# Performance work log

Measured on AMD Instinct MI355X. Metric: run time of the kernel, lower is better.

Reference implementation:

```python
import jax, jax.numpy as jnp
import numpy as np
from jax import lax

DEPTH, HEADS, DH, DIM, M, V, NUM_EMB, D_VQ = 6, 8, 64, 512, 256, 523, 512, 64


def _ln(x, g, b):
    mu = jnp.mean(x, -1, keepdims=True)
    var = jnp.var(x, -1, keepdims=True)
    return (x - mu) * lax.rsqrt(var + 1e-5) * g + b


def _softmax_kernel(data, proj, is_query):
    # FAVOR+ positive softmax features (performer-pytorch softmax_kernel)
    dn = data * (data.shape[-1] ** -0.25)
    dd = jnp.einsum('bhld,md->bhlm', dn, proj)
    diag = 0.5 * jnp.sum(dn * dn, axis=-1, keepdims=True)
    mx = jnp.max(dd, axis=-1, keepdims=True) if is_query else jnp.max(dd)
    return jnp.exp(dd - diag - lax.stop_gradient(mx)) * (proj.shape[0] ** -0.5) + 1e-4


def _causal_linear_attn(qp, kp, v):
    # out_t = qp_t . cumsum_t(kp v^T) / (qp_t . cumsum_t(kp))
    kc = jnp.cumsum(kp, axis=2)
    den = jnp.einsum('bhlm,bhlm->bhl', qp, kc)
    kv = jnp.cumsum(jnp.einsum('bhlm,bhld->bhlmd', kp, v), axis=2)
    return jnp.einsum('bhlm,bhlmd->bhld', qp, kv) / den[..., None]


def _vq_encode(_x, conv1_w, conv1_b, conv2_w, conv2_b, codebook):
    dn = ('NCDHW', 'OIDHW', 'NCDHW')
    h = lax.conv_general_dilated(_x, conv1_w, (2, 2, 2), [(1, 1)] * 3, dimension_numbers=dn)
    h = jax.nn.relu(h + conv1_b[None, :, None, None, None])
    h = lax.conv_general_dilated(h, conv2_w, (2, 2, 2), [(1, 1)] * 3, dimension_numbers=dn)
    h = h + conv2_b[None, :, None, None, None]                 # [N, D, 4,4,4]
    z = jnp.transpose(h, (0, 2, 3, 4, 1))                      # [N, 4,4,4, D]
    flat = z.reshape(-1, z.shape[-1])
    d2 = (jnp.sum(flat * flat, 1, keepdims=True)
          - 2.0 * flat @ codebook.T
          + jnp.sum(codebook * codebook, 1)[None, :])
    inds = jnp.argmin(d2, axis=1).astype(jnp.int32)
    return inds.reshape(z.shape[:4])                           # [N, 4,4,4]


def _performer_loss(seq, tok_emb, pos_emb, proj, ln1_g, ln1_b, wq, wk, wv, wo, bo,
                    ln2_g, ln2_b, ff1_w, ff1_b, ff2_w, ff2_b, lnf_g, lnf_b,
                    logits_w, logits_b):
    inp, tgt = seq[:, :-1], seq[:, 1:]
    b, L = inp.shape
    h = tok_emb[inp] + pos_emb[:L][None]
    split = lambda t: jnp.transpose(t.reshape(b, L, HEADS, DH), (0, 2, 1, 3))
    for l in range(DEPTH):
        x1 = _ln(h, ln1_g[l], ln1_b[l])
        q, k, v = split(x1 @ wq[l]), split(x1 @ wk[l]), split(x1 @ wv[l])
        qp = _softmax_kernel(q, proj[l], True)
        kp = _softmax_kernel(k, proj[l], False)
        o = _causal_linear_attn(qp, kp, v)
        o = jnp.transpose(o, (0, 2, 1, 3)).reshape(b, L, DIM)
        h = h + o @ wo[l] + bo[l]
        x2 = _ln(h, ln2_g[l], ln2_b[l])
        h = h + jax.nn.gelu(x2 @ ff1_w[l] + ff1_b[l]) @ ff2_w[l] + ff2_b[l]
    h = _ln(h, lnf_g, lnf_b)
    logits = h @ logits_w + logits_b
    lp = jax.nn.log_softmax(logits, axis=-1)
    nll = -jnp.take_along_axis(lp, tgt[..., None], axis=-1)[..., 0]
    return jnp.mean(nll)


def setup_inputs() -> dict:
    key = jax.random.key(0)
    ks = jax.random.split(key, 24)
    n = lambda k, sh, s=0.02: (jax.random.normal(k, sh) * s).astype(jnp.float32)
    bs = 16
    return {
        'x': jax.random.normal(ks[0], (bs, 1, 16, 16, 16), jnp.float32),
        'xn': jax.random.normal(ks[1], (bs, 1, 1, 16, 16, 16), jnp.float32),
        'i': jax.random.randint(ks[2], (bs, 3), 0, V, jnp.int32),
        # frozen VQ-VAE
        'conv1_w': n(ks[3], (32, 1, 4, 4, 4), 0.1), 'conv1_b': jnp.zeros((32,), jnp.float32),
        'conv2_w': n(ks[4], (D_VQ, 32, 4, 4, 4), 0.05), 'conv2_b': jnp.zeros((D_VQ,), jnp.float32),
        'codebook': jax.random.normal(ks[5], (NUM_EMB, D_VQ), jnp.float32),
        # FAVOR+ random-feature projections (non-trainable buffer)
        'proj': jax.random.normal(ks[6], (DEPTH, M, DH), jnp.float32),
        # performer params
        'tok_emb': n(ks[7], (V, DIM)), 'pos_emb': n(ks[8], (131, DIM)),
        'ln1_g': jnp.ones((DEPTH, DIM), jnp.float32), 'ln1_b': jnp.zeros((DEPTH, DIM), jnp.float32),
        'wq': n(ks[9], (DEPTH, DIM, DIM)), 'wk': n(ks[10], (DEPTH, DIM, DIM)),
        'wv': n(ks[11], (DEPTH, DIM, DIM)), 'wo': n(ks[12], (DEPTH, DIM, DIM)),
        'bo': jnp.zeros((DEPTH, DIM), jnp.float32),
        'ln2_g': jnp.ones((DEPTH, DIM), jnp.float32), 'ln2_b': jnp.zeros((DEPTH, DIM), jnp.float32),
        'ff1_w': n(ks[13], (DEPTH, DIM, 4 * DIM)), 'ff1_b': jnp.zeros((DEPTH, 4 * DIM), jnp.float32),
        'ff2_w': n(ks[14], (DEPTH, 4 * DIM, DIM)), 'ff2_b': jnp.zeros((DEPTH, DIM), jnp.float32),
        'lnf_g': jnp.ones((DIM,), jnp.float32), 'lnf_b': jnp.zeros((DIM,), jnp.float32),
        'logits_w': n(ks[15], (DIM, V)), 'logits_b': jnp.zeros((V,), jnp.float32),
    }


def reference(x, xn, i, conv1_w, conv1_b, conv2_w, conv2_b, codebook, proj,
              tok_emb, pos_emb, ln1_g, ln1_b, wq, wk, wv, wo, bo, ln2_g, ln2_b,
              ff1_w, ff1_b, ff2_w, ff2_b, lnf_g, lnf_b, logits_w, logits_b):
    bs = x.shape[0]
    _xn = xn.reshape((-1,) + xn.shape[2:])            # (b n) c x y z
    _x = jnp.concatenate([x, _xn], axis=0)
    inds = _vq_encode(_x, conv1_w, conv1_b, conv2_w, conv2_b, codebook)
    inds_i = inds[:bs].reshape(bs, -1)                # b (x y z)
    inds_r = inds[bs:].reshape(bs, -1)                # b (n x y z)
    seq = jnp.concatenate([i.astype(jnp.int32), inds_r, inds_i], axis=1)  # [b, 131]
    return _performer_loss(seq, tok_emb, pos_emb, proj, ln1_g, ln1_b, wq, wk, wv, wo,
                           bo, ln2_g, ln2_b, ff1_w, ff1_b, ff2_w, ff2_b,
                           lnf_g, lnf_b, logits_w, logits_b)
```

## Files before the change

### kernel.cpp

```cpp
#include <hip/hip_runtime.h>

#define SEQL 130
#define LSEQ 131
#define DIMM 512
#define NHEADS 8
#define MF 256
#define VSZ 523
#define NROWS (16*SEQL)
#define NBH (16*NHEADS)
#define NBHL (NBH*SEQL)
#define QSEG 1064960
#define WLAYER 3145728

typedef __attribute__((ext_vector_type(8))) short short8;
typedef __attribute__((ext_vector_type(8))) unsigned short us8;
typedef __attribute__((ext_vector_type(4))) unsigned short us4;
typedef __attribute__((ext_vector_type(4))) float f32x4;

__device__ __forceinline__ unsigned short f2bf(float f){
  unsigned int u = __float_as_uint(f);
  u += 0x7fffu + ((u>>16)&1u);
  return (unsigned short)(u>>16);
}
__device__ __forceinline__ float bf2f(unsigned short h){
  return __uint_as_float(((unsigned int)h)<<16);
}
__device__ __forceinline__ float gelu_f(float x){
  float x3 = x*x*x;
  return 0.5f*x*(1.f+tanhf(0.7978845608028654f*(x+0.044715f*x3)));
}
__device__ __forceinline__ unsigned enc_max(float f){
  unsigned u = __float_as_uint(f);
  return (u & 0x80000000u) ? ~u : (u | 0x80000000u);
}
__device__ __forceinline__ float dec_max(unsigned k){
  unsigned u = (k>>31) ? (k & 0x7fffffffu) : ~k;
  return __uint_as_float(u);
}
__device__ __forceinline__ void gload16(const void* g, void* lds){
  __builtin_amdgcn_global_load_lds(
      (const __attribute__((address_space(1))) void*)g,
      (__attribute__((address_space(3))) void*)lds, 16, 0, 0);
}
__device__ __forceinline__ float blk_sum(float v){
  #pragma unroll
  for(int off=32;off;off>>=1) v += __shfl_xor(v,off);
  __shared__ float tmp_s[4];
  int t=threadIdx.x;
  if((t&63)==0) tmp_s[t>>6]=v;
  __syncthreads();
  v = tmp_s[0]+tmp_s[1]+tmp_s[2]+tmp_s[3];
  __syncthreads();
  return v;
}
__device__ __forceinline__ float blk_max(float v){
  #pragma unroll
  for(int off=32;off;off>>=1) v = fmaxf(v,__shfl_xor(v,off));
  __shared__ float tmp_m[4];
  int t=threadIdx.x;
  if((t&63)==0) tmp_m[t>>6]=v;
  __syncthreads();
  v = fmaxf(fmaxf(tmp_m[0],tmp_m[1]),fmaxf(tmp_m[2],tmp_m[3]));
  __syncthreads();
  return v;
}
__device__ __forceinline__ int tok_at(const int* __restrict__ iarr,
    const int* __restrict__ inds, int b, int p){
  if(p<3)  return iarr[b*3+p];
  if(p<67) return inds[(16+b)*64 + (p-3)];
  return inds[b*64 + (p-67)];
}

__global__ __launch_bounds__(256) void conv1_k(const float* __restrict__ x,
    const float* __restrict__ xn, const float* __restrict__ w,
    const float* __restrict__ bias, float* __restrict__ out){
  int idx = blockIdx.x*256 + threadIdx.x;
  if(idx >= 32*32*8*8*8) return;
  int ow = idx & 7, oh = (idx>>3)&7, od = (idx>>6)&7, oc = (idx>>9)&31, n = idx>>14;
  const float* xp = (n<16) ? (x + n*4096) : (xn + (n-16)*4096);
  const float* wp = w + oc*64;
  float acc = bias[oc];
  #pragma unroll
  for(int kd=0;kd<4;kd++){ int id = od*2-1+kd; if((unsigned)id>=16u) continue;
    #pragma unroll
    for(int kh=0;kh<4;kh++){ int ih = oh*2-1+kh; if((unsigned)ih>=16u) continue;
      #pragma unroll
      for(int kw=0;kw<4;kw++){ int iw = ow*2-1+kw; if((unsigned)iw>=16u) continue;
        acc += xp[(id*16+ih)*16+iw]*wp[(kd*4+kh)*4+kw];
      }}}
  out[idx] = fmaxf(acc,0.f);
}

__global__ __launch_bounds__(256) void cvt8_k(const float* __restrict__ src,
    unsigned short* __restrict__ dst, int n8){
  int i = blockIdx.x*256 + threadIdx.x;
  if(i >= n8) return;
  const float* s = src + (size_t)i*8;
  us8 u;
  #pragma unroll
  for(int j=0;j<8;j++) u[j] = f2bf(s[j]);
  *(us8*)(dst + (size_t)i*8) = u;
}

__global__ __launch_bounds__(256) void im2col_k(const float* __restrict__ c1,
    unsigned short* __restrict__ icol){
  int tid = blockIdx.x*256 + threadIdx.x;
  size_t e0 = (size_t)tid*8;
  int r = (int)(e0 >> 11);
  int k0 = (int)(e0 & 2047);
  int n = r>>6, od = (r>>4)&3, oh = (r>>2)&3, ow = r&3;
  int ic = k0>>6, kd = (k0>>4)&3, kh0 = (k0>>2)&3;
  int id = od*2 - 1 + kd;
  us8 u = {};
  if((unsigned)id < 8u){
    const float* base = c1 + (size_t)(n*32+ic)*512 + id*64;
    #pragma unroll
    for(int j=0;j<8;j++){
      int kh = kh0 + (j>>2), kw = j&3;
      int ih = oh*2 - 1 + kh, iw = ow*2 - 1 + kw;
      float v = 0.f;
      if((unsigned)ih < 8u && (unsigned)iw < 8u) v = base[ih*8 + iw];
      u[j] = f2bf(v);
    }
  }
  *(us8*)(icol + e0) = u;
}

__global__ __launch_bounds__(256) void vq_k(const float* __restrict__ z,
    const float* __restrict__ cb, int* __restrict__ inds){
  int nf = blockIdx.x;
  __shared__ float zs[64];
  int t = threadIdx.x;
  if(t<64) zs[t] = z[(size_t)nf*64 + t];
  __syncthreads();
  float best = 3.0e38f; int bi = 0;
  for(int j=t; j<512; j+=256){
    const float* cr = cb + j*64;
    float dot=0.f, nn=0.f;
    #pragma unroll 8
    for(int d=0;d<64;d++){ float cv=cr[d]; dot += zs[d]*cv; nn += cv*cv; }
    float dist = nn - 2.f*dot;
    if(dist < best){ best=dist; bi=j; }
  }
  #pragma unroll
  for(int off=32;off;off>>=1){
    float ob = __shfl_down(best,off); int oi = __shfl_down(bi,off);
    if(ob<best || (ob==best && oi<bi)){ best=ob; bi=oi; }
  }
  __shared__ float rb[4]; __shared__ int ri[4];
  if((t&63)==0){ rb[t>>6]=best; ri[t>>6]=bi; }
  __syncthreads();
  if(t==0){
    for(int wv=1;wv<4;wv++){ if(rb[wv]<best || (rb[wv]==best && ri[wv]<bi)){ best=rb[wv]; bi=ri[wv]; } }
    inds[nf]=bi;
  }
}

__global__ __launch_bounds__(256) void embed_k(const int* __restrict__ iarr,
    const int* __restrict__ inds, const float* __restrict__ tok,
    const float* __restrict__ pos, float* __restrict__ h){
  int idx = blockIdx.x*256 + threadIdx.x;
  int c = idx & 511; int row = idx >> 9;
  int b = row/SEQL, l = row - b*SEQL;
  int tk = tok_at(iarr, inds, b, l);
  h[idx] = tok[tk*DIMM + c] + pos[l*DIMM + c];
}

__global__ __launch_bounds__(256) void ln_k(const float* __restrict__ in,
    const float* __restrict__ g, const float* __restrict__ bb,
    unsigned short* __restrict__ out){
  int row = blockIdx.x; int t = threadIdx.x;
  const float* xr = in + (size_t)row*DIMM;
  float x0 = xr[t], x1 = xr[t+256];
  float s = x0+x1, ss = x0*x0 + x1*x1;
  #pragma unroll
  for(int off=32;off;off>>=1){ s += __shfl_xor(s,off); ss += __shfl_xor(ss,off); }
  __shared__ float bs[4], bss[4];
  if((t&63)==0){ bs[t>>6]=s; bss[t>>6]=ss; }
  __syncthreads();
  s = bs[0]+bs[1]+bs[2]+bs[3]; ss = bss[0]+bss[1]+bss[2]+bss[3];
  float mu = s*(1.f/512.f);
  float var = ss*(1.f/512.f) - mu*mu;
  float inv = rsqrtf(var + 1e-5f);
  out[(size_t)row*DIMM+t]     = f2bf((x0-mu)*inv*g[t]     + bb[t]);
  out[(size_t)row*DIMM+t+256] = f2bf((x1-mu)*inv*g[t+256] + bb[t+256]);
}

__global__ __launch_bounds__(256) void wprep_k(const float* __restrict__ wq,
    const float* __restrict__ wk, const float* __restrict__ wv,
    const float* __restrict__ wo, const float* __restrict__ ff1,
    const float* __restrict__ ff2, unsigned short* __restrict__ wall,
    unsigned int* __restrict__ gmaxbits){
  int bid0 = blockIdx.x;
  int t = threadIdx.x;
  if(bid0==0 && t<8) gmaxbits[t] = 0u;
  int lyr = bid0 / 3072;
  int bid = bid0 - lyr*3072;
  unsigned short* wl = wall + (size_t)lyr*WLAYER;
  const float* src; unsigned short* dst;
  int n0, k0, srcN, dstK;
  if(bid < 768){
    int nt = bid % 48, kt = bid / 48;
    n0 = nt*32; k0 = kt*32;
    int seg = n0 >> 9;
    src = (seg==0 ? wq : seg==1 ? wk : wv) + (size_t)lyr*262144;
    dst = wl; srcN = 512; dstK = 512;
  } else if(bid < 1024){
    int b2 = bid-768; int nt = b2 % 16, kt = b2 / 16;
    n0 = nt*32; k0 = kt*32; src = wo + (size_t)lyr*262144;
    dst = wl + 786432; srcN = 512; dstK = 512;
  } else if(bid < 2048){
    int b2 = bid-1024; int nt = b2 % 64, kt = b2 / 64;
    n0 = nt*32; k0 = kt*32; src = ff1 + (size_t)lyr*1048576;
    dst = wl + 1048576; srcN = 2048; dstK = 512;
  } else {
    int b2 = bid-2048; int nt = b2 % 16, kt = b2 / 16;
    n0 = nt*32; k0 = kt*32; src = ff2 + (size_t)lyr*1048576;
    dst = wl + 2097152; srcN = 512; dstK = 2048;
  }
  int srcCol0 = (bid < 768) ? (n0 & 0x1ff) : n0;
  __shared__ float tile[32][33];
  int c = t&31, r = t>>5;
  #pragma unroll
  for(int j=0;j<4;j++)
    tile[r+8*j][c] = src[(size_t)(k0+r+8*j)*srcN + srcCol0 + c];
  __syncthreads();
  #pragma unroll
  for(int j=0;j<4;j++){
    int n = n0 + r + 8*j;
    dst[(size_t)n*dstK + k0 + c] = f2bf(tile[c][r+8*j]);
  }
}

__global__ __launch_bounds__(256) void wconv_k(const float* __restrict__ W,
    unsigned short* __restrict__ dst, int K, int N){
  __shared__ float tile[32][33];
  int k0 = blockIdx.y*32, n0 = blockIdx.x*32;
  int t = threadIdx.x; int c = t&31, r = t>>5;
  #pragma unroll
  for(int j=0;j<4;j++){
    int n = n0+c;
    tile[r+8*j][c] = (n<N) ? W[(size_t)(k0+r+8*j)*N + n] : 0.f;
  }
  __syncthreads();
  #pragma unroll
  for(int j=0;j<4;j++){
    int n = n0 + r + 8*j;
    if(n<N) dst[(size_t)n*K + k0 + c] = f2bf(tile[c][r+8*j]);
  }
}

template<int MODE>
__global__ __launch_bounds__(256) void mgemm_k(const unsigned short* __restrict__ A,
    const unsigned short* __restrict__ Bt, const float* __restrict__ bias,
    float* __restrict__ Cf, unsigned short* __restrict__ Cb,
    int M, int N, int K){
  __shared__ __attribute__((aligned(16))) unsigned short As[2][4096];
  __shared__ __attribute__((aligned(16))) unsigned short Bs[2][4096];
  int t = threadIdx.x;
  const int m0 = blockIdx.y*64, n0 = blockIdx.x*64;
  int w = t>>6, l = t&63;
  int wr = w>>1, wc = w&1;
  f32x4 acc[2][2] = {};
  auto stage = [&](unsigned short* Ad, unsigned short* Bd, int k0){
    #pragma unroll
    for(int i=0;i<2;i++){
      int c = w*2 + i;
      int r = c*8 + (l>>3);
      int gc = k0 + (((l&7) ^ (r&7))<<3);
      int ar = m0 + r; if(ar >= M) ar = 0;
      gload16(A + (size_t)ar*K + gc, Ad + c*512);
      int br = n0 + r; if(br >= N) br = 0;
      gload16(Bt + (size_t)br*K + gc, Bd + c*512);
    }
  };
  stage(As[0], Bs[0], 0);
  int NT = K>>6;
  int buf = 0;
  for(int kt=0; kt<NT; kt++){
    __syncthreads();
    if(kt+1 < NT) stage(As[buf^1], Bs[buf^1], (kt+1)*64);
    const unsigned short* Ab = &As[buf][0];
    const unsigned short* Bb = &Bs[buf][0];
    #pragma unroll
    for(int kk=0;kk<2;kk++){
      short8 af[2], bf[2];
      #pragma unroll
      for(int m=0;m<2;m++){
        int row = wr*32 + m*16 + (l&15);
        int slot = kk*4 + (l>>4);
        af[m] = *(const short8*)(Ab + row*64 + ((slot^(row&7))<<3));
      }
      #pragma unroll
      for(int n=0;n<2;n++){
        int col = wc*32 + n*16 + (l&15);
        int slot = kk*4 + (l>>4);
        bf[n] = *(const short8*)(Bb + col*64 + ((slot^(col&7))<<3));
      }
      #pragma unroll
      for(int m=0;m<2;m++)
        #pragma unroll
        for(int n=0;n<2;n++)
          acc[m][n] = __builtin_amdgcn_mfma_f32_16x16x32_bf16(af[m], bf[n], acc[m][n], 0, 0, 0);
    }
    buf ^= 1;
  }
  #pragma unroll
  for(int m=0;m<2;m++){
    #pragma unroll
    for(int n=0;n<2;n++){
      int col = n0 + wc*32 + n*16 + (l&15);
      #pragma unroll
      for(int i=0;i<4;i++){
        int row = m0 + wr*32 + m*16 + (l>>4)*4 + i;
        if(row < M && col < N){
          float v = acc[m][n][i];
          if(MODE==0){
            if(bias) v += bias[col];
            Cf[(size_t)row*N+col] = v;
          } else if(MODE==1){
            v *= (col < 1024) ? 0.35355339059327378f : 1.0f;
            int seg = col>>9, d0 = col&511;
            int hh = d0>>6, d = d0&63;
            int bb = row/SEQL, ll = row - bb*SEQL;
            Cb[(size_t)seg*QSEG + (((size_t)(bb*NHEADS+hh))*SEQL + ll)*64 + d] = f2bf(v);
          } else if(MODE==3){
            v += bias[col];
            Cf[(size_t)row*N+col] += v;
          } else {
            v += bias[col];
            v = gelu_f(v);
            Cb[(size_t)row*N+col] = f2bf(v);
          }
        }
      }
    }
  }
}

template<int ACC>
__global__ __launch_bounds__(256) void mgemm32_k(const unsigned short* __restrict__ A,
    const unsigned short* __restrict__ Bt, const float* __restrict__ bias,
    float* __restrict__ Cf, int N, int K){
  __shared__ __attribute__((aligned(16))) unsigned short As[2][2048];
  __shared__ __attribute__((aligned(16))) unsigned short Bs[2][4096];
  int t = threadIdx.x;
  const int m0 = blockIdx.y*32, n0 = blockIdx.x*64;
  int w = t>>6, l = t&63;
  int wm = w&1, wn2 = w>>1;
  f32x4 acc[2] = {};
  auto stage = [&](unsigned short* Ad, unsigned short* Bd, int k0){
    {
      int c = w;
      int r = c*8 + (l>>3);
      int gc = k0 + (((l&7) ^ (r&7))<<3);
      gload16(A + (size_t)(m0+r)*K + gc, Ad + c*512);
    }
    #pragma unroll
    for(int i=0;i<2;i++){
      int c = w*2 + i;
      int r = c*8 + (l>>3);
      int gc = k0 + (((l&7) ^ (r&7))<<3);
      gload16(Bt + (size_t)(n0+r)*K + gc, Bd + c*512);
    }
  };
  stage(As[0], Bs[0], 0);
  int NT = K>>6;
  int buf = 0;
  for(int kt=0; kt<NT; kt++){
    __syncthreads();
    if(kt+1 < NT) stage(As[buf^1], Bs[buf^1], (kt+1)*64);
    const unsigned short* Ab = &As[buf][0];
    const unsigned short* Bb = &Bs[buf][0];
    #pragma unroll
    for(int kk=0;kk<2;kk++){
      int arow = wm*16 + (l&15);
      int slot = kk*4 + (l>>4);
      short8 af = *(const short8*)(Ab + arow*64 + ((slot^(arow&7))<<3));
      #pragma unroll
      for(int n=0;n<2;n++){
        int col = (wn2*2+n)*16 + (l&15);
        short8 bf = *(const short8*)(Bb + col*64 + ((slot^(col&7))<<3));
        acc[n] = __builtin_amdgcn_mfma_f32_16x16x32_bf16(af, bf, acc[n], 0, 0, 0);
      }
    }
    buf ^= 1;
  }
  #pragma unroll
  for(int n=0;n<2;n++){
    int col = n0 + (wn2*2+n)*16 + (l&15);
    float bv = bias[col];
    #pragma unroll
    for(int i=0;i<4;i++){
      int row = m0 + wm*16 + (l>>4)*4 + i;
      if(ACC) Cf[(size_t)row*N+col] += acc[n][i] + bv;
      else    Cf[(size_t)row*N+col]  = acc[n][i] + bv;
    }
  }
}

__global__ __launch_bounds__(256) void featA_k(const unsigned short* __restrict__ qn,
    const unsigned short* __restrict__ kn, const unsigned short* __restrict__ projl,
    unsigned short* __restrict__ qp, unsigned int* __restrict__ gmaxbits){
  int z = blockIdx.y;
  const unsigned short* dn = z ? kn : qn;
  __shared__ __attribute__((aligned(16))) float uni[32*264];
  __shared__ __attribute__((aligned(16))) unsigned short dns[2048];
  unsigned short* ps = (unsigned short*)uni;
  int t = threadIdx.x;
  int w = t>>6, l = t&63;
  size_t R0 = (size_t)blockIdx.x*32;
  {
    int c = w; int r = c*8 + (l>>3);
    int gc = (((l&7) ^ (r&7))<<3);
    gload16(dn + (R0+r)*64 + gc, dns + c*512);
  }
  #pragma unroll
  for(int i=0;i<8;i++){
    int c = w*8 + i; int r = c*8 + (l>>3);
    int gc = (((l&7) ^ (r&7))<<3);
    gload16(projl + (size_t)r*64 + gc, ps + c*512);
  }
  __syncthreads();
  int rt = w&1, cb = (w>>1)*8;
  f32x4 acc[8] = {};
  #pragma unroll
  for(int kk=0;kk<2;kk++){
    int ar = rt*16 + (l&15);
    int slot = kk*4 + (l>>4);
    short8 a = *(const short8*)(dns + ar*64 + ((slot^(ar&7))<<3));
    #pragma unroll
    for(int ct=0;ct<8;ct++){
      int br = (cb+ct)*16 + (l&15);
      short8 b = *(const short8*)(ps + br*64 + ((slot^(br&7))<<3));
      acc[ct] = __builtin_amdgcn_mfma_f32_16x16x32_bf16(a, b, acc[ct], 0, 0, 0);
    }
  }
  __syncthreads();
  #pragma unroll
  for(int ct=0;ct<8;ct++){
    int col = (cb+ct)*16 + (l&15);
    #pragma unroll
    for(int i=0;i<4;i++){
      int row = rt*16 + (l>>4)*4 + i;
      uni[row*264 + col] = acc[ct][i];
    }
  }
  __syncthreads();
  int r = t>>3, sub = t&7;
  float* rowp = uni + r*264 + sub*32;
  f32x4 v[8];
  #pragma unroll
  for(int jj=0;jj<8;jj++) v[jj] = *(const f32x4*)(rowp + jj*4);
  float m = -3.0e38f;
  #pragma unroll
  for(int jj=0;jj<8;jj++)
    #pragma unroll
    for(int i=0;i<4;i++) m = fmaxf(m, v[jj][i]);
  m = fmaxf(m, __shfl_xor(m,1));
  m = fmaxf(m, __shfl_xor(m,2));
  m = fmaxf(m, __shfl_xor(m,4));
  if(z==0){
    us8 dvu = *(const us8*)(dns + r*64 + ((sub^(r&7))<<3));
    float s2 = 0.f;
    #pragma unroll
    for(int j=0;j<8;j++){ float xx = bf2f(dvu[j]); s2 += xx*xx; }
    s2 += __shfl_xor(s2,1); s2 += __shfl_xor(s2,2); s2 += __shfl_xor(s2,4);
    float ds = 0.5f*s2;
    unsigned short* op = qp + (R0+r)*256 + sub*32;
    #pragma unroll
    for(int jj=0;jj<8;jj++){
      us4 u4;
      #pragma unroll
      for(int i=0;i<4;i++) u4[i] = f2bf(expf(v[jj][i] - ds - m)*0.0625f + 1e-4f);
      *(us4*)(op + jj*4) = u4;
    }
  } else {
    float bm = m;
    bm = fmaxf(bm, __shfl_xor(bm,8));
    bm = fmaxf(bm, __shfl_xor(bm,16));
    bm = fmaxf(bm, __shfl_xor(bm,32));
    __shared__ float wm[4];
    if(l==0) wm[w] = bm;
    __syncthreads();
    if(t==0){
      float g = fmaxf(fmaxf(wm[0],wm[1]),fmaxf(wm[2],wm[3]));
      atomicMax(gmaxbits, enc_max(g));
    }
  }
}

__global__ __launch_bounds__(256) void featB_k(const unsigned short* __restrict__ kn,
    const unsigned short* __restrict__ projl, const unsigned int* __restrict__ gmaxbits,
    unsigned short* __restrict__ kp){
  __shared__ __attribute__((aligned(16))) float uni[32*264];
  __shared__ __attribute__((aligned(16))) unsigned short dns[2048];
  unsigned short* ps = (unsigned short*)uni;
  int t = threadIdx.x;
  int w = t>>6, l = t&63;
  size_t R0 = (size_t)blockIdx.x*32;
  {
    int c = w; int r = c*8 + (l>>3);
    int gc = (((l&7) ^ (r&7))<<3);
    gload16(kn + (R0+r)*64 + gc, dns + c*512);
  }
  #pragma unroll
  for(int i=0;i<8;i++){
    int c = w*8 + i; int r = c*8 + (l>>3);
    int gc = (((l&7) ^ (r&7))<<3);
    gload16(projl + (size_t)r*64 + gc, ps + c*512);
  }
  __syncthreads();
  int rt = w&1, cb = (w>>1)*8;
  f32x4 acc[8] = {};
  #pragma unroll
  for(int kk=0;kk<2;kk++){
    int ar = rt*16 + (l&15);
    int slot = kk*4 + (l>>4);
    short8 a = *(const short8*)(dns + ar*64 + ((slot^(ar&7))<<3));
    #pragma unroll
    for(int ct=0;ct<8;ct++){
      int br = (cb+ct)*16 + (l&15);
      short8 b = *(const short8*)(ps + br*64 + ((slot^(br&7))<<3));
      acc[ct] = __builtin_amdgcn_mfma_f32_16x16x32_bf16(a, b, acc[ct], 0, 0, 0);
    }
  }
  __syncthreads();
  #pragma unroll
  for(int ct=0;ct<8;ct++){
    int col = (cb+ct)*16 + (l&15);
    #pragma unroll
    for(int i=0;i<4;i++){
      int row = rt*16 + (l>>4)*4 + i;
      uni[row*264 + col] = acc[ct][i];
    }
  }
  __syncthreads();
  float g = dec_max(gmaxbits[0]);
  int r = t>>3, sub = t&7;
  us8 dvu = *(const us8*)(dns + r*64 + ((sub^(r&7))<<3));
  float s2 = 0.f;
  #pragma unroll
  for(int j=0;j<8;j++){ float xx = bf2f(dvu[j]); s2 += xx*xx; }
  s2 += __shfl_xor(s2,1); s2 += __shfl_xor(s2,2); s2 += __shfl_xor(s2,4);
  float ds = 0.5f*s2;
  float* rowp = uni + r*264 + sub*32;
  unsigned short* op = kp + (R0+r)*256 + sub*32;
  #pragma unroll
  for(int jj=0;jj<8;jj++){
    f32x4 v = *(const f32x4*)(rowp + jj*4);
    us4 u4;
    #pragma unroll
    for(int i=0;i<4;i++) u4[i] = f2bf(expf(v[i] - ds - g)*0.0625f + 1e-4f);
    *(us4*)(op + jj*4) = u4;
  }
}

__global__ __launch_bounds__(256) void attn_k(const unsigned short* __restrict__ qp,
    const unsigned short* __restrict__ kp, const unsigned short* __restrict__ vn,
    unsigned short* __restrict__ ob){
  int qt = blockIdx.x, bh = blockIdx.y;
  int b = bh>>3, hh = bh&7;
  __shared__ __attribute__((aligned(16))) unsigned short qs[8192];
  __shared__ __attribute__((aligned(16))) unsigned short ks[8192];
  __shared__ __attribute__((aligned(16))) unsigned short VTs[64*34];
  __shared__ __attribute__((aligned(16))) unsigned short Sb[32*36];
  __shared__ float dens[2][32];
  int t = threadIdx.x;
  int w = t>>6, l = t&63;
  int qh = w>>1, nc = w&1;
  #pragma unroll
  for(int i=0;i<4;i++){
    int c = w*4 + i; int r = (c<<1) + (l>>5); int sl = l&31;
    int gc = ((sl ^ (r&7))<<3);
    int gr = qt*32 + r; if(gr >= SEQL) gr = 0;
    gload16(qp + ((size_t)bh*SEQL + gr)*256 + gc, qs + c*512);
  }
  if(t<64) dens[t>>5][t&31] = 0.f;
  f32x4 oacc[2] = {};
  for(int kt=0; kt<=qt; kt++){
    __syncthreads();
    #pragma unroll
    for(int i=0;i<4;i++){
      int c = w*4 + i; int r = (c<<1) + (l>>5); int sl = l&31;
      int gc = ((sl ^ (r&7))<<3);
      int gk = kt*32 + r; if(gk >= SEQL) gk = 0;
      gload16(kp + ((size_t)bh*SEQL + gk)*256 + gc, ks + c*512);
    }
    {
      int rr = t>>3, od = (t&7)*8;
      int gk = kt*32 + rr;
      us8 uv = {};
      if(gk < SEQL) uv = *(const us8*)(vn + ((size_t)bh*SEQL + gk)*64 + od);
      #pragma unroll
      for(int j=0;j<8;j++) VTs[(od+j)*34 + rr] = uv[j];
    }
    __syncthreads();
    f32x4 sacc = {};
    #pragma unroll
    for(int kk=0;kk<8;kk++){
      int ar = qh*16 + (l&15); int slot = kk*4 + (l>>4);
      short8 a = *(const short8*)(qs + ar*256 + ((slot^(ar&7))<<3));
      int br = nc*16 + (l&15);
      short8 bb2 = *(const short8*)(ks + br*256 + ((slot^(br&7))<<3));
      sacc = __builtin_amdgcn_mfma_f32_16x16x32_bf16(a, bb2, sacc, 0, 0, 0);
    }
    int scol = nc*16 + (l&15);
    int gcol = kt*32 + scol;
    float dp[4];
    #pragma unroll
    for(int i=0;i<4;i++){
      int sr = qh*16 + (l>>4)*4 + i;
      int grw = qt*32 + sr;
      float v2 = sacc[i];
      if(gcol > grw) v2 = 0.f;
      Sb[sr*36 + scol] = f2bf(v2);
      dp[i] = v2;
    }
    #pragma unroll
    for(int off=1;off<16;off<<=1)
      #pragma unroll
      for(int i=0;i<4;i++) dp[i] += __shfl_xor(dp[i], off);
    if((l&15)==0){
      #pragma unroll
      for(int i=0;i<4;i++) dens[nc][qh*16 + (l>>4)*4 + i] += dp[i];
    }
    __syncthreads();
    short8 a2 = *(const short8*)(Sb + (qh*16 + (l&15))*36 + (l>>4)*8);
    #pragma unroll
    for(int n2=0;n2<2;n2++){
      int d = nc*32 + n2*16 + (l&15);
      short8 b2 = *(const short8*)(VTs + d*34 + (l>>4)*8);
      oacc[n2] = __builtin_amdgcn_mfma_f32_16x16x32_bf16(a2, b2, oacc[n2], 0, 0, 0);
    }
  }
  __syncthreads();
  #pragma unroll
  for(int n2=0;n2<2;n2++){
    int d = nc*32 + n2*16 + (l&15);
    #pragma unroll
    for(int i=0;i<4;i++){
      int rit = qh*16 + (l>>4)*4 + i;
      int gr = qt*32 + rit;
      if(gr < SEQL){
        float inv = 1.f/(dens[0][rit] + dens[1][rit]);
        ob[((size_t)(b*SEQL+gr))*DIMM + hh*64 + d] = f2bf(oacc[n2][i]*inv);
      }
    }
  }
}

__global__ __launch_bounds__(256) void loss_k(const float* __restrict__ logits,
    const int* __restrict__ iarr, const int* __restrict__ inds,
    float* __restrict__ rnll){
  int row = blockIdx.x; int t = threadIdx.x;
  const float* lr = logits + (size_t)row*VSZ;
  float m = -3.0e38f;
  for(int j=t;j<VSZ;j+=256) m = fmaxf(m, lr[j]);
  m = blk_max(m);
  float s = 0.f;
  for(int j=t;j<VSZ;j+=256) s += expf(lr[j]-m);
  s = blk_sum(s);
  if(t==0){
    int b = row/SEQL, l = row - b*SEQL;
    int tgt = tok_at(iarr, inds, b, l+1);
    rnll[row] = (m + logf(s)) - lr[tgt];
  }
}

__global__ __launch_bounds__(256) void fin_k(const float* __restrict__ rnll,
    float* __restrict__ out){
  int t = threadIdx.x;
  float s = 0.f;
  for(int i=t;i<NROWS;i+=256) s += rnll[i];
  s = blk_sum(s);
  if(t==0) out[0] = s/(float)NROWS;
}

extern "C" void kernel_launch(void* const* d_in, const int* in_sizes, int n_in,
                              void* d_out, int out_size, void* d_ws, size_t ws_size,
                              hipStream_t stream){
  (void)in_sizes; (void)n_in; (void)out_size; (void)ws_size;
  const float* x        = (const float*)d_in[0];
  const float* xn       = (const float*)d_in[1];
  const int*   iarr     = (const int*)  d_in[2];
  const float* conv1_w  = (const float*)d_in[3];
  const float* conv1_b  = (const float*)d_in[4];
  const float* conv2_w  = (const float*)d_in[5];
  const float* conv2_b  = (const float*)d_in[6];
  const float* codebook = (const float*)d_in[7];
  const float* proj     = (const float*)d_in[8];
  const float* tok_emb  = (const float*)d_in[9];
  const float* pos_emb  = (const float*)d_in[10];
  const float* ln1_g    = (const float*)d_in[11];
  const float* ln1_b    = (const float*)d_in[12];
  const float* wq       = (const float*)d_in[13];
  const float* wk       = (const float*)d_in[14];
  const float* wv       = (const float*)d_in[15];
  const float* wo       = (const float*)d_in[16];
  const float* bo       = (const float*)d_in[17];
  const float* ln2_g    = (const float*)d_in[18];
  const float* ln2_b    = (const float*)d_in[19];
  const float* ff1_w    = (const float*)d_in[20];
  const float* ff1_b    = (const float*)d_in[21];
  const float* ff2_w    = (const float*)d_in[22];
  const float* ff2_b    = (const float*)d_in[23];
  const float* lnf_g    = (const float*)d_in[24];
  const float* lnf_b    = (const float*)d_in[25];
  const float* logits_w = (const float*)d_in[26];
  const float* logits_b = (const float*)d_in[27];

  float* wsf = (float*)d_ws;
  size_t off = 0;
  unsigned short* qp_bf = (unsigned short*)(wsf + off); off += 2129920;
  unsigned short* kp_bf = (unsigned short*)(wsf + off); off += 2129920;
  float* h = wsf + off; off += 1064960;
  unsigned short* x1b = (unsigned short*)(wsf + off); off += 532480;
  unsigned short* qkvb = (unsigned short*)(wsf + off); off += 1597440;
  unsigned short* ob  = (unsigned short*)(wsf + off); off += 532480;
  unsigned short* projb = (unsigned short*)(wsf + off); off += 49152;
  unsigned short* wall  = (unsigned short*)(wsf + off); off += 9437184;
  unsigned short* logt  = (unsigned short*)(wsf + off); off += 133888;
  unsigned short* ffmid = (unsigned short*)(wsf + off); off += 2129920;
  float* logits = wsf + off; off += 1087840;
  int* inds = (int*)(wsf + off); off += 2048;
  unsigned int* gmaxbits = (unsigned int*)(wsf + off); off += 64;
  float* rnll = wsf + off; off += 2112;

  float* c1 = logits;
  unsigned short* icol = ffmid;
  float* zbuf = (float*)qp_bf;
  unsigned short* cw2b = (unsigned short*)kp_bf;

  unsigned short* qnb = qkvb;
  unsigned short* knb = qkvb + QSEG;
  unsigned short* vnb = qkvb + 2*QSEG;

  conv1_k<<<2048,256,0,stream>>>(x, xn, conv1_w, conv1_b, c1);
  cvt8_k<<<64,256,0,stream>>>(conv2_w, cw2b, 16384);
  im2col_k<<<2048,256,0,stream>>>(c1, icol);
  mgemm32_k<0><<<dim3(1,64),256,0,stream>>>(icol, cw2b, conv2_b, zbuf, 64, 2048);
  vq_k<<<2048,256,0,stream>>>(zbuf, codebook, inds);
  embed_k<<<(NROWS*DIMM)/256,256,0,stream>>>(iarr, inds, tok_emb, pos_emb, h);
  cvt8_k<<<48,256,0,stream>>>(proj, projb, 12288);
  wconv_k<<<dim3(17,16),256,0,stream>>>(logits_w, logt, 512, 523);
  wprep_k<<<18432,256,0,stream>>>(wq, wk, wv, wo, ff1_w, ff2_w, wall, gmaxbits);

  for(int l=0;l<6;l++){
    unsigned short* wl    = wall + (size_t)l*WLAYER;
    unsigned short* wqkvt = wl;
    unsigned short* wot   = wl + 786432;
    unsigned short* ff1t  = wl + 1048576;
    unsigned short* ff2t  = wl + 2097152;
    ln_k<<<NROWS,256,0,stream>>>(h, ln1_g+l*DIMM, ln1_b+l*DIMM, x1b);
    mgemm_k<1><<<dim3(24,33),256,0,stream>>>(x1b, wqkvt, nullptr, nullptr, qkvb, NROWS, 1536, DIMM);
    featA_k<<<dim3(520,2),256,0,stream>>>(qnb, knb, projb + l*16384, qp_bf, gmaxbits + l);
    featB_k<<<520,256,0,stream>>>(knb, projb + l*16384, gmaxbits + l, kp_bf);
    attn_k<<<dim3(5,NBH),256,0,stream>>>(qp_bf, kp_bf, vnb, ob);
    mgemm32_k<1><<<dim3(8,65),256,0,stream>>>(ob, wot, bo+l*DIMM, h, DIMM, DIMM);
    ln_k<<<NROWS,256,0,stream>>>(h, ln2_g+l*DIMM, ln2_b+l*DIMM, x1b);
    mgemm_k<4><<<dim3(32,33),256,0,stream>>>(x1b, ff1t, ff1_b+l*2048, nullptr, ffmid, NROWS, 2048, DIMM);
    mgemm32_k<1><<<dim3(8,65),256,0,stream>>>(ffmid, ff2t, ff2_b+l*DIMM, h, DIMM, 2048);
  }

  ln_k<<<NROWS,256,0,stream>>>(h, lnf_g, lnf_b, x1b);
  mgemm_k<0><<<dim3(9,33),256,0,stream>>>(x1b, logt, logits_b, logits, nullptr, NROWS, VSZ, DIMM);
  loss_k<<<NROWS,256,0,stream>>>(logits, iarr, inds, rnll);
  fin_k<<<1,256,0,stream>>>(rnll, (float*)d_out);
}
```

Before: 749.4 us.

## Enlarge GEMM tiles to 128x128/128x64 and vectorize row-per-wave layernorm

Replaces the 64x64 GEMM with 128x128 and 128x64 tiled variants, giving each wave a larger register accumulator tile. This raises data reuse per LDS load and cuts the block count. LayerNorm now handles one row per wave with vectorized loads and stores and no shared-memory reduction. The cost is fewer blocks for a small M=2080, which can leave CUs idle on a 256-CU part, plus extra padded work at the M edge (2080 over 17 tiles of 128).

```diff
diff --git a/kernel.cpp b/kernel.cpp
--- a/kernel.cpp
+++ b/kernel.cpp
@@ -169,21 +169,27 @@
 __global__ __launch_bounds__(256) void ln_k(const float* __restrict__ in,
     const float* __restrict__ g, const float* __restrict__ bb,
     unsigned short* __restrict__ out){
-  int row = blockIdx.x; int t = threadIdx.x;
-  const float* xr = in + (size_t)row*DIMM;
-  float x0 = xr[t], x1 = xr[t+256];
-  float s = x0+x1, ss = x0*x0 + x1*x1;
+  int w = threadIdx.x>>6, l = threadIdx.x&63;
+  int row = blockIdx.x*4 + w;
+  const float* xr = in + (size_t)row*DIMM + l*8;
+  f32x4 v0 = *(const f32x4*)xr;
+  f32x4 v1 = *(const f32x4*)(xr+4);
+  float s = v0[0]+v0[1]+v0[2]+v0[3]+v1[0]+v1[1]+v1[2]+v1[3];
+  float ss = v0[0]*v0[0]+v0[1]*v0[1]+v0[2]*v0[2]+v0[3]*v0[3]
+           + v1[0]*v1[0]+v1[1]*v1[1]+v1[2]*v1[2]+v1[3]*v1[3];
   #pragma unroll
   for(int off=32;off;off>>=1){ s += __shfl_xor(s,off); ss += __shfl_xor(ss,off); }
-  __shared__ float bs[4], bss[4];
-  if((t&63)==0){ bs[t>>6]=s; bss[t>>6]=ss; }
-  __syncthreads();
-  s = bs[0]+bs[1]+bs[2]+bs[3]; ss = bss[0]+bss[1]+bss[2]+bss[3];
   float mu = s*(1.f/512.f);
   float var = ss*(1.f/512.f) - mu*mu;
   float inv = rsqrtf(var + 1e-5f);
-  out[(size_t)row*DIMM+t]     = f2bf((x0-mu)*inv*g[t]     + bb[t]);
-  out[(size_t)row*DIMM+t+256] = f2bf((x1-mu)*inv*g[t+256] + bb[t+256]);
+  const float* gp = g + l*8; const float* bp = bb + l*8;
+  us8 u;
+  #pragma unroll
+  for(int j=0;j<4;j++){
+    u[j]   = f2bf((v0[j]-mu)*inv*gp[j]   + bp[j]);
+    u[4+j] = f2bf((v1[j]-mu)*inv*gp[4+j] + bp[4+j]);
+  }
+  *(us8*)(out + (size_t)row*DIMM + l*8) = u;
 }
 
 __global__ __launch_bounds__(256) void wprep_k(const float* __restrict__ wq,
@@ -251,21 +257,20 @@
 }
 
 template<int MODE>
-__global__ __launch_bounds__(256) void mgemm_k(const unsigned short* __restrict__ A,
+__global__ __launch_bounds__(256) void gemm128x128_k(const unsigned short* __restrict__ A,
     const unsigned short* __restrict__ Bt, const float* __restrict__ bias,
     float* __restrict__ Cf, unsigned short* __restrict__ Cb,
     int M, int N, int K){
-  __shared__ __attribute__((aligned(16))) unsigned short As[2][4096];
-  __shared__ __attribute__((aligned(16))) unsigned short Bs[2][4096];
-  int t = threadIdx.x;
-  const int m0 = blockIdx.y*64, n0 = blockIdx.x*64;
-  int w = t>>6, l = t&63;
+  __shared__ __attribute__((aligned(16))) unsigned short As[2][8192];
+  __shared__ __attribute__((aligned(16))) unsigned short Bs[2][8192];
+  int t = threadIdx.x, w = t>>6, l = t&63;
+  const int m0 = blockIdx.y*128, n0 = blockIdx.x*128;
   int wr = w>>1, wc = w&1;
-  f32x4 acc[2][2] = {};
+  f32x4 acc[4][4] = {};
   auto stage = [&](unsigned short* Ad, unsigned short* Bd, int k0){
     #pragma unroll
-    for(int i=0;i<2;i++){
-      int c = w*2 + i;
+    for(int i=0;i<4;i++){
+      int c = w*4 + i;
       int r = c*8 + (l>>3);
       int gc = k0 + (((l&7) ^ (r&7))<<3);
       int ar = m0 + r; if(ar >= M) ar = 0;
@@ -275,63 +280,132 @@
     }
   };
   stage(As[0], Bs[0], 0);
-  int NT = K>>6;
-  int buf = 0;
-  for(int kt=0; kt<NT; kt++){
+  int NTk = K>>6, buf = 0;
+  for(int kt=0; kt<NTk; kt++){
     __syncthreads();
-    if(kt+1 < NT) stage(As[buf^1], Bs[buf^1], (kt+1)*64);
+    if(kt+1 < NTk) stage(As[buf^1], Bs[buf^1], (kt+1)*64);
     const unsigned short* Ab = &As[buf][0];
     const unsigned short* Bb = &Bs[buf][0];
     #pragma unroll
     for(int kk=0;kk<2;kk++){
-      short8 af[2], bf[2];
-      #pragma unroll
-      for(int m=0;m<2;m++){
-        int row = wr*32 + m*16 + (l&15);
+      short8 af[4], bf[4];
+      #pragma unroll
+      for(int m=0;m<4;m++){
+        int row = wr*64 + m*16 + (l&15);
         int slot = kk*4 + (l>>4);
         af[m] = *(const short8*)(Ab + row*64 + ((slot^(row&7))<<3));
       }
       #pragma unroll
-      for(int n=0;n<2;n++){
-        int col = wc*32 + n*16 + (l&15);
+      for(int n=0;n<4;n++){
+        int col = wc*64 + n*16 + (l&15);
         int slot = kk*4 + (l>>4);
         bf[n] = *(const short8*)(Bb + col*64 + ((slot^(col&7))<<3));
       }
       #pragma unroll
-      for(int m=0;m<2;m++)
+      for(int m=0;m<4;m++)
         #pragma unroll
-        for(int n=0;n<2;n++)
+        for(int n=0;n<4;n++)
           acc[m][n] = __builtin_amdgcn_mfma_f32_16x16x32_bf16(af[m], bf[n], acc[m][n], 0, 0, 0);
     }
     buf ^= 1;
   }
   #pragma unroll
-  for(int m=0;m<2;m++){
-    #pragma unroll
-    for(int n=0;n<2;n++){
-      int col = n0 + wc*32 + n*16 + (l&15);
+  for(int m=0;m<4;m++){
+    #pragma unroll
+    for(int n=0;n<4;n++){
+      int col = n0 + wc*64 + n*16 + (l&15);
       #pragma unroll
       for(int i=0;i<4;i++){
-        int row = m0 + wr*32 + m*16 + (l>>4)*4 + i;
+        int row = m0 + wr*64 + m*16 + (l>>4)*4 + i;
         if(row < M && col < N){
           float v = acc[m][n][i];
-          if(MODE==0){
-            if(bias) v += bias[col];
-            Cf[(size_t)row*N+col] = v;
-          } else if(MODE==1){
+          if(MODE==1){
             v *= (col < 1024) ? 0.35355339059327378f : 1.0f;
             int seg = col>>9, d0 = col&511;
             int hh = d0>>6, d = d0&63;
             int bb = row/SEQL, ll = row - bb*SEQL;
             Cb[(size_t)seg*QSEG + (((size_t)(bb*NHEADS+hh))*SEQL + ll)*64 + d] = f2bf(v);
-          } else if(MODE==3){
-            v += bias[col];
-            Cf[(size_t)row*N+col] += v;
           } else {
             v += bias[col];
             v = gelu_f(v);
             Cb[(size_t)row*N+col] = f2bf(v);
           }
+        }
+      }
+    }
+  }
+}
+
+template<int MODE>
+__global__ __launch_bounds__(256) void gemm128x64_k(const unsigned short* __restrict__ A,
+    const unsigned short* __restrict__ Bt, const float* __restrict__ bias,
+    float* __restrict__ Cf, int M, int N, int K){
+  __shared__ __attribute__((aligned(16))) unsigned short As[2][8192];
+  __shared__ __attribute__((aligned(16))) unsigned short Bs[2][4096];
+  int t = threadIdx.x, w = t>>6, l = t&63;
+  const int m0 = blockIdx.y*128, n0 = blockIdx.x*64;
+  f32x4 acc[2][4] = {};
+  auto stage = [&](unsigned short* Ad, unsigned short* Bd, int k0){
+    #pragma unroll
+    for(int i=0;i<4;i++){
+      int c = w*4 + i;
+      int r = c*8 + (l>>3);
+      int gc = k0 + (((l&7) ^ (r&7))<<3);
+      int ar = m0 + r; if(ar >= M) ar = 0;
+      gload16(A + (size_t)ar*K + gc, Ad + c*512);
+    }
+    #pragma unroll
+    for(int i=0;i<2;i++){
+      int c = w*2 + i;
+      int r = c*8 + (l>>3);
+      int gc = k0 + (((l&7) ^ (r&7))<<3);
+      int br = n0 + r; if(br >= N) br = 0;
+      gload16(Bt + (size_t)br*K + gc, Bd + c*512);
+    }
+  };
+  stage(As[0], Bs[0], 0);
+  int NTk = K>>6, buf = 0;
+  for(int kt=0; kt<NTk; kt++){
+    __syncthreads();
+    if(kt+1 < NTk) stage(As[buf^1], Bs[buf^1], (kt+1)*64);
+    const unsigned short* Ab = &As[buf][0];
+    const unsigned short* Bb = &Bs[buf][0];
+    #pragma unroll
+    for(int kk=0;kk<2;kk++){
+      short8 af[2], bf[4];
+      #pragma unroll
+      for(int m=0;m<2;m++){
+        int row = w*32 + m*16 + (l&15);
+        int slot = kk*4 + (l>>4);
+        af[m] = *(const short8*)(Ab + row*64 + ((slot^(row&7))<<3));
+      }
+      #pragma unroll
+      for(int n=0;n<4;n++){
+        int col = n*16 + (l&15);
+        int slot = kk*4 + (l>>4);
+        bf[n] = *(const short8*)(Bb + col*64 + ((slot^(col&7))<<3));
+      }
+      #pragma unroll
+      for(int m=0;m<2;m++)
+        #pragma unroll
+        for(int n=0;n<4;n++)
+          acc[m][n] = __builtin_amdgcn_mfma_f32_16x16x32_bf16(af[m], bf[n], acc[m][n], 0, 0, 0);
+    }
+    buf ^= 1;
+  }
+  #pragma unroll
+  for(int m=0;m<2;m++){
+    #pragma unroll
+    for(int n=0;n<4;n++){
+      int col = n0 + n*16 + (l&15);
+      if(col >= N) continue;
+      float bv = bias[col];
+      #pragma unroll
+      for(int i=0;i<4;i++){
+        int row = m0 + w*32 + m*16 + (l>>4)*4 + i;
+        if(row < M){
+          if(MODE==3) Cf[(size_t)row*N+col] += acc[m][n][i] + bv;
+          else        Cf[(size_t)row*N+col]  = acc[m][n][i] + bv;
         }
       }
     }
@@ -752,19 +826,19 @@
     unsigned short* wot   = wl + 786432;
     unsigned short* ff1t  = wl + 1048576;
     unsigned short* ff2t  = wl + 2097152;
-    ln_k<<<NROWS,256,0,stream>>>(h, ln1_g+l*DIMM, ln1_b+l*DIMM, x1b);
-    mgemm_k<1><<<dim3(24,33),256,0,stream>>>(x1b, wqkvt, nullptr, nullptr, qkvb, NROWS, 1536, DIMM);
+    ln_k<<<520,256,0,stream>>>(h, ln1_g+l*DIMM, ln1_b+l*DIMM, x1b);
+    gemm128x128_k<1><<<dim3(12,17),256,0,stream>>>(x1b, wqkvt, nullptr, nullptr, qkvb, NROWS, 1536, DIMM);
     featA_k<<<dim3(520,2),256,0,stream>>>(qnb, knb, projb + l*16384, qp_bf, gmaxbits + l);
     featB_k<<<520,256,0,stream>>>(knb, projb + l*16384, gmaxbits + l, kp_bf);
     attn_k<<<dim3(5,NBH),256,0,stream>>>(qp_bf, kp_bf, vnb, ob);
-    mgemm32_k<1><<<dim3(8,65),256,0,stream>>>(ob, wot, bo+l*DIMM, h, DIMM, DIMM);
-    ln_k<<<NROWS,256,0,stream>>>(h, ln2_g+l*DIMM, ln2_b+l*DIMM, x1b);
-    mgemm_k<4><<<dim3(32,33),256,0,stream>>>(x1b, ff1t, ff1_b+l*2048, nullptr, ffmid, NROWS, 2048, DIMM);
-    mgemm32_k<1><<<dim3(8,65),256,0,stream>>>(ffmid, ff2t, ff2_b+l*DIMM, h, DIMM, 2048);
-  }
-
-  ln_k<<<NROWS,256,0,stream>>>(h, lnf_g, lnf_b, x1b);
-  mgemm_k<0><<<dim3(9,33),256,0,stream>>>(x1b, logt, logits_b, logits, nullptr, NROWS, VSZ, DIMM);
+    gemm128x64_k<3><<<dim3(8,17),256,0,stream>>>(ob, wot, bo+l*DIMM, h, NROWS, DIMM, DIMM);
+    ln_k<<<520,256,0,stream>>>(h, ln2_g+l*DIMM, ln2_b+l*DIMM, x1b);
+    gemm128x128_k<4><<<dim3(16,17),256,0,stream>>>(x1b, ff1t, ff1_b+l*2048, nullptr, ffmid, NROWS, 2048, DIMM);
+    gemm128x64_k<3><<<dim3(8,17),256,0,stream>>>(ffmid, ff2t, ff2_b+l*DIMM, h, NROWS, DIMM, 2048);
+  }
+
+  ln_k<<<520,256,0,stream>>>(h, lnf_g, lnf_b, x1b);
+  gemm128x64_k<0><<<dim3(9,17),256,0,stream>>>(x1b, logt, logits_b, logits, NROWS, VSZ, DIMM);
   loss_k<<<NROWS,256,0,stream>>>(logits, iarr, inds, rnll);
   fin_k<<<1,256,0,stream>>>(rnll, (float*)d_out);
 }
```

Result: slower. 940.7 us (+25.5%).
